# Optimization experiments

Measured on AMD Instinct MI355X. Metric: run time of the kernel, lower is better.

The kernel has to match this reference:

```python
import jax, jax.numpy as jnp
import numpy as np

B, CIN, COUT, H, W, K = 4, 64, 64, 128, 128, 3
KK = K * K


def setup_inputs() -> dict:
    key = jax.random.key(0)
    k = jax.random.split(key, 7)
    return {
        "input_feat": jax.random.normal(k[0], (B, CIN, H, W), jnp.float32),
        "inter": jax.random.normal(k[1], (B, CIN, H, W), jnp.float32),
        "fea": jax.random.normal(k[2], (B, 4 * CIN, 1, 1), jnp.float32),
        "weight": jax.random.uniform(k[3], (COUT, CIN, K, K), jnp.float32, -1.0, 1.0) / np.float32(np.sqrt(CIN * KK)),
        "bias": jnp.zeros((COUT,), jnp.float32),
        # conv_offset_mask params (torch zero-inits; small random values used so offsets/masks are non-trivial)
        "com_w": jax.random.normal(k[4], (3 * KK, CIN, K, K), jnp.float32) * 0.01,
        "com_b": jnp.zeros((3 * KK,), jnp.float32),
        "c1_w": jax.random.normal(k[5], (COUT, 4 * CIN), jnp.float32) / np.float32(np.sqrt(4 * CIN)),
        "c2_w": jax.random.normal(k[6], (COUT, COUT), jnp.float32) / np.float32(np.sqrt(COUT)),
    }


def reference(input_feat, inter, fea, weight, bias, com_w, com_b, c1_w, c2_w):
    b, c, h, w = input_feat.shape
    # offset/mask prediction: 3x3 conv, stride 1, pad 1 -> [b, 3*KK, h, w]
    om = jax.lax.conv_general_dilated(inter, com_w, (1, 1), ((1, 1), (1, 1)),
                                      dimension_numbers=("NCHW", "OIHW", "NCHW"))
    om = om + com_b[None, :, None, None]
    offset = jnp.concatenate([om[:, :KK], om[:, KK:2 * KK]], axis=1)  # [b, 2*KK, h, w]
    mask = jax.nn.sigmoid(om[:, 2 * KK:])                              # [b, KK, h, w]
    dy, dx = offset[:, 0::2], offset[:, 1::2]                          # mmcv interleaved (y, x) per tap

    # dynamic per-sample weight modulation (Cout == Cin, fea scales the in-channel axis)
    fvec = jnp.einsum('oc,bc->bo', c1_w, fea[:, :, 0, 0])              # [b, COUT]
    wdyn = weight[None] * fvec[:, None, :, None, None]                 # [b, COUT, CIN, K, K]

    # sampling coordinates: base grid (stride=1, pad=1, dil=1) + learned offsets
    ky = jnp.repeat(jnp.arange(K), K).astype(jnp.float32)              # [KK]
    kx = jnp.tile(jnp.arange(K), K).astype(jnp.float32)
    base_y = jnp.arange(h, dtype=jnp.float32)[None, :, None] - 1.0 + ky[:, None, None]  # [KK, h, 1]
    base_x = jnp.arange(w, dtype=jnp.float32)[None, None, :] - 1.0 + kx[:, None, None]  # [KK, 1, w]
    ys = base_y[None] + dy                                             # [b, KK, h, w]
    xs = base_x[None] + dx

    y0f = jnp.floor(ys); x0f = jnp.floor(xs)
    ly = ys - y0f; lx = xs - x0f
    y0 = y0f.astype(jnp.int32); x0 = x0f.astype(jnp.int32)
    xf = input_feat.reshape(b, c, h * w)

    def gather(yi, xi, wgt):
        valid = (yi >= 0) & (yi < h) & (xi >= 0) & (xi < w)
        idx = jnp.clip(yi, 0, h - 1) * w + jnp.clip(xi, 0, w - 1)      # [b, KK, h, w]
        v = jnp.take_along_axis(xf, idx.reshape(b, 1, -1), axis=2).reshape(b, c, KK, h, w)
        return v * (wgt * valid)[:, None]

    val = (gather(y0, x0, (1 - ly) * (1 - lx)) + gather(y0, x0 + 1, (1 - ly) * lx)
           + gather(y0 + 1, x0, ly * (1 - lx)) + gather(y0 + 1, x0 + 1, ly * lx))
    val = val * mask[:, None]                                          # modulated samples [b, c, KK, h, w]

    out = jnp.einsum('bocp,bcphw->bohw', wdyn.reshape(b, COUT, c, KK), val) + bias[None, :, None, None]
    return jnp.einsum('oc,bchw->bohw', c2_w, out)                      # c2: 1x1 conv, no bias
```

## Files before the change

kernel.cpp:

```cpp
#include <hip/hip_runtime.h>
#include <math.h>

#define BB 4
#define CIN 64
#define COUT 64
#define HH 128
#define WW 128
#define HW (HH*WW)

typedef __attribute__((ext_vector_type(8))) short short8;
typedef __attribute__((ext_vector_type(4))) float f32x4;
typedef __attribute__((ext_vector_type(4))) unsigned int uint4v;

static __device__ __forceinline__ unsigned short f2bf(float f) {
    unsigned int u = __builtin_bit_cast(unsigned int, f);
    u += 0x7fffu + ((u >> 16) & 1u);
    return (unsigned short)(u >> 16);
}
static __device__ __forceinline__ float bf2f(unsigned short h) {
    unsigned int u = ((unsigned int)h) << 16;
    return __builtin_bit_cast(float, u);
}

__global__ __launch_bounds__(256) void prep_kernel(
        const float* __restrict__ com_w, const float* __restrict__ c2w,
        const float* __restrict__ bias,
        unsigned short* __restrict__ wk2, float* __restrict__ bias2) {
    int id = blockIdx.x, tid = threadIdx.x;
    if (id < 80) {
        int i = id*256 + tid;
        int k = i & 31, oc = (i >> 5) & 31;
        int cc5 = i >> 10;
        int cg = cc5 / 5, ch = cc5 % 5;
        int tap = ch*2 + (k >> 4);
        int c = cg*16 + (k & 15);
        float v = 0.f;
        if (tap < 9 && oc < 27) v = com_w[((size_t)oc*64 + c)*9 + tap];
        wk2[i] = f2bf(v);
    } else if (tid < COUT) {
        float s2 = 0.f;
        for (int o = 0; o < COUT; ++o) s2 += c2w[tid*COUT + o] * bias[o];
        bias2[tid] = s2;
    }
}

static __device__ __forceinline__ void transpose_body(
        const float* __restrict__ srcb, unsigned short* __restrict__ dstb,
        int tb, int tid, float* lt ) {
    int b = tb >> 8;
    int px0 = (tb & 255) * 64;
    const float* src = srcb + (size_t)b*CIN*HW + px0;
    for (int i = tid; i < 4096; i += 256) {
        int c = i >> 6, px = i & 63;
        lt[c*65 + px] = src[(size_t)c*HW + px];
    }
    __syncthreads();
    int q = tid & 3, px = tid >> 2;
    unsigned short* dst = dstb + ((size_t)b*HW + px0 + px)*64 + q*16;
    #pragma unroll
    for (int s = 0; s < 2; ++s) {
        short8 pk;
        #pragma unroll
        for (int j = 0; j < 8; ++j)
            pk[j] = (short)f2bf(lt[(q*16 + s*8 + j)*65 + px]);
        *(short8*)(dst + s*8) = pk;
    }
}

static __device__ __forceinline__ void w2_body(
        int wid, int tid, const float* __restrict__ weight,
        const float* __restrict__ c2w, const float* __restrict__ c1w,
        const float* __restrict__ fea,
        unsigned short* __restrict__ w2b, float* c2s, float* wcol) {
    int o2 = tid & 63, ci = tid >> 6;
    int lane = tid & 63;
    int bp = wid >> 4;
    int c_base = (wid & 15)*4;
    int p = bp % 9, b = bp / 9;
    int c = c_base + ci;

    float part = 0.f;
    #pragma unroll
    for (int s = 0; s < 4; ++s)
        part += c1w[c*(4*CIN) + lane + s*64] * fea[b*(4*CIN) + lane + s*64];
    #pragma unroll
    for (int off = 32; off; off >>= 1) part += __shfl_down(part, off);
    float fv = __shfl(part, 0);

    for (int idx = tid; idx < 4096; idx += 256) {
        int o2r = idx >> 6, oc = idx & 63;
        c2s[oc*65 + o2r] = c2w[idx];
    }
    {
        int o = tid & 63, cw = tid >> 6;
        wcol[cw*64 + o] = weight[(o*CIN + (c_base + cw))*9 + p];
    }
    __syncthreads();
    float s = 0.f;
    #pragma unroll 8
    for (int o = 0; o < COUT; ++o) s += c2s[o*65 + o2] * wcol[ci*64 + o];
    w2b[(size_t)bp*4096 + o2*64 + (c ^ ((o2 & 7) << 3))] = f2bf(s * fv);
}

static __device__ __forceinline__ void conv_lds_body(
        int id, int tid, const float* __restrict__ inter,
        const unsigned short* __restrict__ wk2, const float* __restrict__ com_b,
        float* __restrict__ om, float* smemf) {
    unsigned short* til = (unsigned short*)smemf;
    int b  = id >> 7;
    int t7 = id & 127;
    int by = t7 >> 3;
    int bx = t7 & 7;
    int x0 = bx*16, y0 = by*8;
    int lane = tid & 63, wv = tid >> 6;
    int nn = lane & 15, qq = lane >> 4;

    if (tid < 24) til[180*24 + tid] = 0;

    int scl = tid & 15, scc = tid >> 4;
    int sgx  = x0 + scc - 1;
    int sgxc = max(sgx, 0);
    float sfx = ((unsigned)sgx < WW) ? 1.f : 0.f;

    f32x4 acc[2][2];
    #pragma unroll
    for (int nt = 0; nt < 2; ++nt)
        #pragma unroll
        for (int mh = 0; mh < 2; ++mh)
            #pragma unroll
            for (int j = 0; j < 4; ++j) acc[nt][mh][j] = 0.f;

    for (int cg = 0; cg < 4; ++cg) {
        __syncthreads();
        const float* I = inter + ((size_t)(b*CIN + cg*16))*HW;

        {
            const float* colp = I + (size_t)scl*HW + sgxc;
            unsigned short* tp = til + scc*24 + scl;
            #pragma unroll
            for (int r = 0; r < 10; ++r) {
                int gy  = y0 + r - 1;
                int gyc = min(max(gy, 0), HH-1);
                float m = ((unsigned)gy < HH) ? sfx : 0.f;
                float v = colp[(size_t)gyc*WW] * m;
                tp[r*(18*24)] = f2bf(v);
            }
        }
        #pragma unroll
        for (int k = 0; k < 2; ++k) {
            int i = k*256 + tid;
            if (i < 320) {
                int cl  = i & 15;
                int ccb = (i >> 4) & 1;
                int r   = i >> 5;
                int gx  = x0 + 15 + ccb;
                int gy  = y0 + r - 1;
                int gxc = min(gx, WW-1);
                int gyc = min(max(gy, 0), HH-1);
                float m = (((unsigned)gy < HH) && ((unsigned)gx < WW)) ? 1.f : 0.f;
                float v = I[(size_t)cl*HW + gyc*WW + gxc] * m;
                til[(r*18 + 16 + ccb)*24 + cl] = f2bf(v);
            }
        }
        __syncthreads();

        #pragma unroll
        for (int ch = 0; ch < 5; ++ch) {
            short8 a0 = *(const short8*)(wk2 +
                (((size_t)(cg*5 + ch)*32 + nn)*32 + qq*8));
            short8 a1 = *(const short8*)(wk2 +
                (((size_t)(cg*5 + ch)*32 + 16 + nn)*32 + qq*8));
            int tap = ch*2 + (qq >> 1);
            #pragma unroll
            for (int nt = 0; nt < 2; ++nt) {
                int row = wv*2 + nt;
                int px_idx;
                if (tap > 8) px_idx = 180;
                else {
                    int ky = tap/3, kx = tap%3;
                    px_idx = (row + ky)*18 + (nn + kx);
                }
                short8 bfr = *(const short8*)(til + px_idx*24 + (qq&1)*8);
                acc[nt][0] = __builtin_amdgcn_mfma_f32_16x16x32_bf16(
                                 a0, bfr, acc[nt][0], 0, 0, 0);
                acc[nt][1] = __builtin_amdgcn_mfma_f32_16x16x32_bf16(
                                 a1, bfr, acc[nt][1], 0, 0, 0);
            }
        }
    }

    float* op = om + (size_t)b*27*HW;
    #pragma unroll
    for (int nt = 0; nt < 2; ++nt) {
        int pix = (y0 + wv*2 + nt)*WW + x0 + nn;
        #pragma unroll
        for (int mh = 0; mh < 2; ++mh)
            #pragma unroll
            for (int j = 0; j < 4; ++j) {
                int oc = mh*16 + qq*4 + j;
                if (oc < 27)
                    op[(size_t)oc*HW + pix] = acc[nt][mh][j] + com_b[oc];
            }
    }
}

__global__ __launch_bounds__(256) void main2_kernel(
        const float* __restrict__ input_feat,
        const float* __restrict__ inter,
        const unsigned short* __restrict__ wk2,
        const float* __restrict__ com_b,
        const float* __restrict__ weight,
        const float* __restrict__ c2w,
        const float* __restrict__ c1w,
        const float* __restrict__ fea,
        float* __restrict__ om, unsigned short* __restrict__ w2b,
        unsigned short* __restrict__ fT) {
    __shared__ __align__(16) float smem[4416];
    int id = blockIdx.x, tid = threadIdx.x;
    if (id < 512)        conv_lds_body(id, tid, inter, wk2, com_b, om, smem);
    else if (id < 1088)  w2_body(id - 512, tid, weight, c2w, c1w, fea, w2b,
                                 smem, smem + 64*65);
    else                 transpose_body(input_feat, fT, id - 1088, tid, smem);
}

__global__ __launch_bounds__(256) void dcn_main_kernel(
        const unsigned short* __restrict__ fT,
        const unsigned short* __restrict__ w2b,
        const float* __restrict__ bias2,
        const float* __restrict__ om,
        float* __restrict__ out) {
    __shared__ __align__(16) unsigned short aT[2][4096];
    int id = blockIdx.x;
    int xcd = id & 7;
    int jj  = id >> 3;
    int b   = xcd >> 1;
    int y   = jj & 127;
    int xq  = ((xcd & 1) << 1) | (jj >> 7);

    int t = threadIdx.x;
    int lane = t & 63, wv = t >> 6;
    int strip = wv >> 1, kh = wv & 1;
    int nn = lane & 15, qq = lane >> 4;
    int px0 = xq*32 + strip*16;
    int x = px0 + nn;
    int pix = y*WW + x;
    const unsigned short* Fb = fT + (size_t)b*HW*64;
    const float* omb = om + (size_t)b*27*HW;
    const unsigned short* w2src = w2b + (size_t)(b*9)*4096;
    int co = kh*32 + qq*8;

    char* aTc0 = (char*)aT[0];
    char* aTc1 = (char*)aT[1];
    int stOff = wv*2048 + lane*16;
    int rsw   = (nn & 7) << 4;
    int rbase = kh*64 + qq*16;

    f32x4 acc[4];
    #pragma unroll
    for (int mt = 0; mt < 4; ++mt)
        #pragma unroll
        for (int j = 0; j < 4; ++j)
            acc[mt][j] = kh ? bias2[mt*16 + qq*4 + j] : 0.f;

    {
        const char* s = (const char*)w2src;
        __builtin_amdgcn_global_load_lds(
            (const __attribute__((address_space(1))) void*)(s + stOff),
            (__attribute__((address_space(3))) void*)(aTc0 + wv*2048),
            16, 0, 0);
        __builtin_amdgcn_global_load_lds(
            (const __attribute__((address_space(1))) void*)(s + stOff + 1024),
            (__attribute__((address_space(3))) void*)(aTc0 + wv*2048 + 1024),
            16, 0, 0);
    }

    float omy = omb[pix];
    float omx = omb[(size_t)HW + pix];
    float omm = omb[(size_t)18*HW + pix];
    __syncthreads();

    #pragma unroll
    for (int p = 0; p < 9; ++p) {
        char* bufR = (p & 1) ? aTc1 : aTc0;
        char* bufW = (p & 1) ? aTc0 : aTc1;

        if (p < 8) {
            const char* s = (const char*)(w2src + (size_t)(p + 1)*4096);
            __builtin_amdgcn_global_load_lds(
                (const __attribute__((address_space(1))) void*)(s + stOff),
                (__attribute__((address_space(3))) void*)(bufW + wv*2048),
                16, 0, 0);
            __builtin_amdgcn_global_load_lds(
                (const __attribute__((address_space(1))) void*)(s + stOff + 1024),
                (__attribute__((address_space(3))) void*)(bufW + wv*2048 + 1024),
                16, 0, 0);
        }

        short8 afr[4];
        #pragma unroll
        for (int mt = 0; mt < 4; ++mt)
            afr[mt] = *(const short8*)(bufR +
                          (((mt*16 + nn)*128 + rbase) ^ rsw));

        float mv = 1.f / (1.f + expf(-omm));
        float ysv = (float)(y - 1 + p/3) + omy;
        float xsv = (float)(x - 1 + p%3) + omx;
        float y0f = floorf(ysv), x0f = floorf(xsv);
        float ly = ysv - y0f, lx = xsv - x0f;
        int y0 = (int)y0f, x0i = (int)x0f;
        int y1 = y0 + 1, x1 = x0i + 1;
        float vy0 = (y0 >= 0 && y0 < HH) ? 1.f : 0.f;
        float vy1 = (y1 >= 0 && y1 < HH) ? 1.f : 0.f;
        float vx0 = (x0i >= 0 && x0i < WW) ? 1.f : 0.f;
        float vx1 = (x1 >= 0 && x1 < WW) ? 1.f : 0.f;
        float w00 = (1.f-ly)*(1.f-lx)*mv * vy0*vx0;
        float w01 = (1.f-ly)*lx      *mv * vy0*vx1;
        float w10 = ly      *(1.f-lx)*mv * vy1*vx0;
        float w11 = ly      *lx      *mv * vy1*vx1;
        int y0c = min(max(y0,0),HH-1), y1c = min(max(y1,0),HH-1);
        int x0c = min(max(x0i,0),WW-1), x1c = min(max(x1,0),WW-1);
        int i00 = y0c*WW + x0c, i01 = y0c*WW + x1c;
        int i10 = y1c*WW + x0c, i11 = y1c*WW + x1c;

        if (p < 8) {
            omy = omb[(size_t)(2*p+2)*HW + pix];
            omx = omb[(size_t)(2*p+3)*HW + pix];
            omm = omb[(size_t)(19+p )*HW + pix];
        }

        short8 c00 = *(const short8*)(Fb + (size_t)i00*64 + co);
        short8 c01 = *(const short8*)(Fb + (size_t)i01*64 + co);
        short8 c10 = *(const short8*)(Fb + (size_t)i10*64 + co);
        short8 c11 = *(const short8*)(Fb + (size_t)i11*64 + co);

        unsigned int pw[4];
        #pragma unroll
        for (int jp = 0; jp < 4; ++jp) {
            float v0 = w00*bf2f((unsigned short)c00[2*jp])
                     + w01*bf2f((unsigned short)c01[2*jp])
                     + w10*bf2f((unsigned short)c10[2*jp])
                     + w11*bf2f((unsigned short)c11[2*jp]);
            float v1 = w00*bf2f((unsigned short)c00[2*jp+1])
                     + w01*bf2f((unsigned short)c01[2*jp+1])
                     + w10*bf2f((unsigned short)c10[2*jp+1])
                     + w11*bf2f((unsigned short)c11[2*jp+1]);
            pw[jp] = (unsigned int)f2bf(v0) | ((unsigned int)f2bf(v1) << 16);
        }
        uint4v u4 = {pw[0], pw[1], pw[2], pw[3]};
        short8 bfr = __builtin_bit_cast(short8, u4);

        #pragma unroll
        for (int mt = 0; mt < 4; ++mt)
            acc[mt] = __builtin_amdgcn_mfma_f32_16x16x32_bf16(
                          afr[mt], bfr, acc[mt], 0, 0, 0);

        __syncthreads();
    }

    float* red = (float*)aTc1;
    if (kh == 0) {
        #pragma unroll
        for (int mt = 0; mt < 4; ++mt)
            #pragma unroll
            for (int j = 0; j < 4; ++j)
                red[(mt*4 + j)*128 + strip*64 + lane] = acc[mt][j];
    }
    __syncthreads();
    if (kh == 1) {
        float* outp = out + (size_t)b*COUT*HW + (size_t)y*WW + px0 + nn;
        #pragma unroll
        for (int mt = 0; mt < 4; ++mt)
            #pragma unroll
            for (int j = 0; j < 4; ++j)
                outp[(size_t)(mt*16 + qq*4 + j)*HW] =
                    acc[mt][j] + red[(mt*4 + j)*128 + strip*64 + lane];
    }
}

extern "C" void kernel_launch(void* const* d_in, const int* in_sizes, int n_in,
                              void* d_out, int out_size, void* d_ws, size_t ws_size,
                              hipStream_t stream) {
    const float* input_feat = (const float*)d_in[0];
    const float* inter      = (const float*)d_in[1];
    const float* fea        = (const float*)d_in[2];
    const float* weight     = (const float*)d_in[3];
    const float* bias       = (const float*)d_in[4];
    const float* com_w      = (const float*)d_in[5];
    const float* com_b      = (const float*)d_in[6];
    const float* c1w        = (const float*)d_in[7];
    const float* c2w        = (const float*)d_in[8];
    float* out = (float*)d_out;

    float* ws    = (float*)d_ws;
    float* bias2 = ws + 256;
    unsigned short* w2b = (unsigned short*)(ws + 512);
    float* om    = ws + 512 + 73728;
    unsigned short* wk2 = (unsigned short*)(om + 1769472);
    unsigned short* fT  = wk2 + 20480;

    prep_kernel<<<81, 256, 0, stream>>>(com_w, c2w, bias, wk2, bias2);
    main2_kernel<<<2112, 256, 0, stream>>>(input_feat, inter, wk2, com_b,
                                           weight, c2w, c1w, fea, om, w2b, fT);
    dcn_main_kernel<<<2048, 256, 0, stream>>>(fT, w2b, bias2, om, out);
}
```

Before: 151.4 us.

## Load MFMA weight fragments directly from global memory instead of LDS double-buffering

Drops the LDS double-buffered staging of per-tap weight tiles, which used global_load_lds and a barrier every tap. Each wave now reads its A fragments directly from global memory (L1/L2-resident) with an unswizzled layout, and the prep kernel writes weights unswizzled to match. This removes nine block barriers and the LDS traffic. The cost is redundant global/L2 loads per wave and the loss of prefetch overlap.

New measurement: 177.6 us. 1.17x slower.

```diff
diff --git a/kernel.cpp b/kernel.cpp
--- a/kernel.cpp
+++ b/kernel.cpp
@@ -99,7 +99,7 @@
     float s = 0.f;
     #pragma unroll 8
     for (int o = 0; o < COUT; ++o) s += c2s[o*65 + o2] * wcol[ci*64 + o];
-    w2b[(size_t)bp*4096 + o2*64 + (c ^ ((o2 & 7) << 3))] = f2bf(s * fv);
+    w2b[(size_t)bp*4096 + o2*64 + c] = f2bf(s * fv);
 }
 
 static __device__ __forceinline__ void conv_lds_body(
@@ -229,7 +229,7 @@
         const float* __restrict__ bias2,
         const float* __restrict__ om,
         float* __restrict__ out) {
-    __shared__ __align__(16) unsigned short aT[2][4096];
+    __shared__ float red[16*2*64];
     int id = blockIdx.x;
     int xcd = id & 7;
     int jj  = id >> 3;
@@ -246,14 +246,8 @@
     int pix = y*WW + x;
     const unsigned short* Fb = fT + (size_t)b*HW*64;
     const float* omb = om + (size_t)b*27*HW;
-    const unsigned short* w2src = w2b + (size_t)(b*9)*4096;
+    const unsigned short* w2p = w2b + (size_t)(b*9)*4096 + kh*32 + qq*8;
     int co = kh*32 + qq*8;
-
-    char* aTc0 = (char*)aT[0];
-    char* aTc1 = (char*)aT[1];
-    int stOff = wv*2048 + lane*16;
-    int rsw   = (nn & 7) << 4;
-    int rbase = kh*64 + qq*16;
 
     f32x4 acc[4];
     #pragma unroll
@@ -261,46 +255,17 @@
         #pragma unroll
         for (int j = 0; j < 4; ++j)
             acc[mt][j] = kh ? bias2[mt*16 + qq*4 + j] : 0.f;
-
-    {
-        const char* s = (const char*)w2src;
-        __builtin_amdgcn_global_load_lds(
-            (const __attribute__((address_space(1))) void*)(s + stOff),
-            (__attribute__((address_space(3))) void*)(aTc0 + wv*2048),
-            16, 0, 0);
-        __builtin_amdgcn_global_load_lds(
-            (const __attribute__((address_space(1))) void*)(s + stOff + 1024),
-            (__attribute__((address_space(3))) void*)(aTc0 + wv*2048 + 1024),
-            16, 0, 0);
-    }
 
     float omy = omb[pix];
     float omx = omb[(size_t)HW + pix];
     float omm = omb[(size_t)18*HW + pix];
-    __syncthreads();
 
     #pragma unroll
     for (int p = 0; p < 9; ++p) {
-        char* bufR = (p & 1) ? aTc1 : aTc0;
-        char* bufW = (p & 1) ? aTc0 : aTc1;
-
-        if (p < 8) {
-            const char* s = (const char*)(w2src + (size_t)(p + 1)*4096);
-            __builtin_amdgcn_global_load_lds(
-                (const __attribute__((address_space(1))) void*)(s + stOff),
-                (__attribute__((address_space(3))) void*)(bufW + wv*2048),
-                16, 0, 0);
-            __builtin_amdgcn_global_load_lds(
-                (const __attribute__((address_space(1))) void*)(s + stOff + 1024),
-                (__attribute__((address_space(3))) void*)(bufW + wv*2048 + 1024),
-                16, 0, 0);
-        }
-
         short8 afr[4];
         #pragma unroll
         for (int mt = 0; mt < 4; ++mt)
-            afr[mt] = *(const short8*)(bufR +
-                          (((mt*16 + nn)*128 + rbase) ^ rsw));
+            afr[mt] = *(const short8*)(w2p + (size_t)p*4096 + (mt*16 + nn)*64);
 
         float mv = 1.f / (1.f + expf(-omm));
         float ysv = (float)(y - 1 + p/3) + omy;
@@ -353,11 +318,8 @@
         for (int mt = 0; mt < 4; ++mt)
             acc[mt] = __builtin_amdgcn_mfma_f32_16x16x32_bf16(
                           afr[mt], bfr, acc[mt], 0, 0, 0);
-
-        __syncthreads();
-    }
-
-    float* red = (float*)aTc1;
+    }
+
     if (kh == 0) {
         #pragma unroll
         for (int mt = 0; mt < 4; ++mt)
```
